# Kernel optimization log

Measured on AMD Instinct MI355X. Metric: run time of the kernel, lower is better.

## Reference

```python
import jax, jax.numpy as jnp
import numpy as np
from jax import lax

EPS_BN = 1e-5
EPS_LN = 1e-5


def setup_inputs() -> dict:
    key = jax.random.key(0)
    ks = jax.random.split(key, 10)
    B, Cin, H, W = 32, 512, 56, 56
    Cout, Cr = 128, 128 // 16  # CBAM reduction 16
    x = jax.random.normal(ks[0], (B, Cin, H, W), dtype=jnp.float32)
    w_proj = jax.random.normal(ks[1], (Cout, Cin), dtype=jnp.float32) * 0.02
    bn_g = jnp.ones((Cout,), jnp.float32)
    bn_b = jnp.zeros((Cout,), jnp.float32)
    bn_m = jax.random.normal(ks[2], (Cout,), dtype=jnp.float32) * 0.1
    bn_v = jax.random.uniform(ks[3], (Cout,), dtype=jnp.float32, minval=0.5, maxval=1.5)
    ca_w1 = jax.random.normal(ks[4], (Cr, Cout), dtype=jnp.float32) * 0.05
    ca_w2 = jax.random.normal(ks[5], (Cout, Cr), dtype=jnp.float32) * 0.05
    sa_w = jax.random.normal(ks[6], (1, 2, 7, 7), dtype=jnp.float32) * 0.05
    ln_g = jnp.ones((Cout,), jnp.float32)
    ln_b = jnp.zeros((Cout,), jnp.float32)
    return dict(x=x, w_proj=w_proj, bn_g=bn_g, bn_b=bn_b, bn_m=bn_m, bn_v=bn_v,
                ca_w1=ca_w1, ca_w2=ca_w2, sa_w=sa_w, ln_g=ln_g, ln_b=ln_b)


def _cbam(x, ca_w1, ca_w2, sa_w):
    # Channel attention: shared MLP on GAP and GMP over spatial dims
    avg = x.mean(axis=(2, 3))  # [B, C]
    mx = x.max(axis=(2, 3))    # [B, C]
    mlp = lambda p: jnp.einsum('cr,br->bc', ca_w2, jax.nn.relu(jnp.einsum('rc,bc->br', ca_w1, p)))
    ca = jax.nn.sigmoid(mlp(avg) + mlp(mx))  # [B, C]
    x = x * ca[:, :, None, None]
    # Spatial attention: channel-wise avg/max -> 7x7 conv -> sigmoid
    s = jnp.stack([x.mean(axis=1), x.max(axis=1)], axis=1)  # [B, 2, H, W]
    sa = lax.conv_general_dilated(s, sa_w, (1, 1), [(3, 3), (3, 3)],
                                  dimension_numbers=('NCHW', 'OIHW', 'NCHW'))
    return x * jax.nn.sigmoid(sa)


def reference(x, w_proj, bn_g, bn_b, bn_m, bn_v, ca_w1, ca_w2, sa_w, ln_g, ln_b):
    # 1x1 conv (no bias) as GEMM over channels
    h = jnp.einsum('bchw,oc->bohw', x, w_proj)
    # BatchNorm (inference) + SiLU
    scale = (bn_g / jnp.sqrt(bn_v + EPS_BN))[None, :, None, None]
    shift = (bn_b - bn_m * bn_g / jnp.sqrt(bn_v + EPS_BN))[None, :, None, None]
    h = h * scale + shift
    h = h * jax.nn.sigmoid(h)  # SiLU
    # CBAM with residual
    y = _cbam(h, ca_w1, ca_w2, sa_w) + h
    # GAP over spatial -> LayerNorm over channels
    y = y.mean(axis=(2, 3))  # [B, C]
    mu = y.mean(axis=-1, keepdims=True)
    var = ((y - mu) ** 2).mean(axis=-1, keepdims=True)
    return (y - mu) / jnp.sqrt(var + EPS_LN) * ln_g + ln_b
```

## Files before the change

kernel.cpp:

```cpp
#include <hip/hip_runtime.h>
#include <hip/hip_bf16.h>

typedef __bf16 bf16x8 __attribute__((ext_vector_type(8)));
typedef float f32x4 __attribute__((ext_vector_type(4)));

#define NB 32
#define CIN 512
#define COUT 128
#define NP 3136
#define WIMG 56

__device__ __forceinline__ unsigned fenc(float f) {
    unsigned u = __float_as_uint(f);
    return (u & 0x80000000u) ? ~u : (u | 0x80000000u);
}
__device__ __forceinline__ float fdec(unsigned e) {
    unsigned u = (e & 0x80000000u) ? (e ^ 0x80000000u) : ~e;
    return __uint_as_float(u);
}
__device__ __forceinline__ float bflo(unsigned u) { return __uint_as_float(u << 16); }
__device__ __forceinline__ float bfhi(unsigned u) { return __uint_as_float(u & 0xffff0000u); }

__device__ __forceinline__ unsigned cvt2_fp8(float a, float b) {
    unsigned r;
    asm volatile("v_cvt_pk_fp8_f32 %0, %1, %2" : "=&v"(r) : "v"(a), "v"(b));
    return r & 0xffffu;
}
__device__ __forceinline__ unsigned pack4_fp8(unsigned u01, unsigned u23) {
    unsigned lo = cvt2_fp8(bflo(u01), bfhi(u01));
    unsigned hi = cvt2_fp8(bflo(u23), bfhi(u23));
    return lo | (hi << 16);
}
__device__ __forceinline__ float fp8_entry(int v) {
    unsigned s = (v >> 7) & 1, e = (v >> 3) & 15, m = v & 7;
    if (e) return __uint_as_float((s << 31) | ((e + 120) << 23) | (m << 20));
    float f = (float)m * 0x1p-9f;
    return s ? -f : f;
}

__device__ __forceinline__ void lds_barrier() {
    asm volatile("s_waitcnt lgkmcnt(0)" ::: "memory");
    __builtin_amdgcn_s_barrier();
    __builtin_amdgcn_sched_barrier(0);
}

__global__ __launch_bounds__(256) void k_wcvt(const float* __restrict__ wp,
                                              ushort* __restrict__ wb,
                                              unsigned* __restrict__ zero8k)
{
    int i = blockIdx.x * 256 + threadIdx.x;
    if (i < 2 * NB * COUT) zero8k[i] = 0u;
    float4 f = *(const float4*)(wp + i * 4);
    ushort4 u;
    __bf16 b0 = (__bf16)f.x, b1 = (__bf16)f.y, b2 = (__bf16)f.z, b3 = (__bf16)f.w;
    u.x = *(ushort*)&b0; u.y = *(ushort*)&b1; u.z = *(ushort*)&b2; u.w = *(ushort*)&b3;
    *(ushort4*)(wb + i * 4) = u;
}

__global__ __launch_bounds__(512, 6) void k_main(
    const float* __restrict__ x, const ushort* __restrict__ wb,
    const float* __restrict__ bn_g, const float* __restrict__ bn_b,
    const float* __restrict__ bn_m, const float* __restrict__ bn_v,
    uchar* __restrict__ hout, float* __restrict__ sumh, unsigned* __restrict__ mxenc)
{
    __shared__ __align__(16) ushort Xs[2][64 * 64];
    __shared__ __align__(16) ushort Ws[2][128 * 64];
    __shared__ float bnss[256];
    __shared__ float redS[2][COUT];
    __shared__ float redM[2][COUT];

    const int bid  = blockIdx.x;
    const int swz  = (bid & 7) * 196 + (bid >> 3);
    const int t    = threadIdx.x;
    const int b    = swz / 49;
    const int p0   = (swz % 49) * 64;
    const int lane = t & 63;
    const int l15  = lane & 15;
    const int lg   = lane >> 4;
    const int w    = t >> 6;
    const int wm   = w >> 1;
    const int wn   = w & 1;

    if (t < COUT) {
        float sc = bn_g[t] * rsqrtf(bn_v[t] + 1e-5f);
        bnss[t]        = sc;
        bnss[t + COUT] = bn_b[t] - bn_m[t] * sc;
    }

    const int pr = t & 63;
    const int kg = t >> 6;
    const float* xb = x + ((size_t)b * CIN) * NP + p0 + pr;
    const int xbyte = pr * 128 + ((kg * 16) ^ ((pr & 7) << 4));

    const int ow = t >> 2, kq = t & 3;
    const ushort* wsrc = wb + ow * CIN + kq * 16;
    const int wbyte0 = ow * 128 + ((kq * 32) ^ ((ow & 7) << 4));
    const int wbyte1 = ow * 128 + ((kq * 32 + 16) ^ ((ow & 7) << 4));

    f32x4 acc[2][2];
#pragma unroll
    for (int mf = 0; mf < 2; ++mf)
#pragma unroll
        for (int nf = 0; nf < 2; ++nf) acc[mf][nf] = (f32x4){0.f, 0.f, 0.f, 0.f};

    float ldx[2][8];
    uint4 ldw0, ldw1;

#pragma unroll
    for (int j = 0; j < 8; ++j) {
        ldx[0][j] = xb[(kg * 8 + j) * NP];
        ldx[1][j] = xb[(64 + kg * 8 + j) * NP];
    }
    ldw0 = *(const uint4*)(wsrc);
    ldw1 = *(const uint4*)(wsrc + 8);
    {
        bf16x8 v8;
#pragma unroll
        for (int j = 0; j < 8; ++j) v8[j] = (__bf16)ldx[0][j];
        *(bf16x8*)((char*)Xs[0] + xbyte) = v8;
        *(uint4*)((char*)Ws[0] + wbyte0) = ldw0;
        *(uint4*)((char*)Ws[0] + wbyte1) = ldw1;
    }

#pragma unroll
    for (int kc = 0; kc < 8; ++kc) {
        lds_barrier();
        if (kc < 6) {
#pragma unroll
            for (int j = 0; j < 8; ++j)
                ldx[kc & 1][j] = xb[((kc + 2) * 64 + kg * 8 + j) * NP];
        }
        if (kc < 7) {
            ldw0 = *(const uint4*)(wsrc + (kc + 1) * 64);
            ldw1 = *(const uint4*)(wsrc + (kc + 1) * 64 + 8);
        }
#pragma unroll
        for (int ks = 0; ks < 2; ++ks) {
            bf16x8 af[2], bfr[2];
#pragma unroll
            for (int mf = 0; mf < 2; ++mf) {
                int o = wm * 32 + mf * 16 + l15;
                af[mf] = *(const bf16x8*)((const char*)Ws[kc & 1]
                          + o * 128 + ((ks * 64 + lg * 16) ^ ((o & 7) << 4)));
            }
#pragma unroll
            for (int nf = 0; nf < 2; ++nf) {
                int p = wn * 32 + nf * 16 + l15;
                bfr[nf] = *(const bf16x8*)((const char*)Xs[kc & 1]
                           + p * 128 + ((ks * 64 + lg * 16) ^ ((p & 7) << 4)));
            }
#pragma unroll
            for (int mf = 0; mf < 2; ++mf)
#pragma unroll
                for (int nf = 0; nf < 2; ++nf)
                    acc[mf][nf] = __builtin_amdgcn_mfma_f32_16x16x32_bf16(
                        af[mf], bfr[nf], acc[mf][nf], 0, 0, 0);
        }
        if (kc < 7) {
            bf16x8 v8;
#pragma unroll
            for (int j = 0; j < 8; ++j) v8[j] = (__bf16)ldx[(kc + 1) & 1][j];
            *(bf16x8*)((char*)Xs[(kc + 1) & 1] + xbyte) = v8;
            *(uint4*)((char*)Ws[(kc + 1) & 1] + wbyte0) = ldw0;
            *(uint4*)((char*)Ws[(kc + 1) & 1] + wbyte1) = ldw1;
        }
    }

    __syncthreads();
    ushort* Hs = (ushort*)Xs;
#pragma unroll
    for (int mf = 0; mf < 2; ++mf) {
#pragma unroll
        for (int reg = 0; reg < 4; ++reg) {
            int o = wm * 32 + mf * 16 + lg * 4 + reg;
            float sc = bnss[o], sh = bnss[o + COUT];
            float s_ = 0.f, m_ = -1e30f;
#pragma unroll
            for (int nf = 0; nf < 2; ++nf) {
                float d    = acc[mf][nf][reg];
                float hval = d * sc + sh;
                hval       = hval / (1.f + __expf(-hval));
                s_ += hval;
                m_ = fmaxf(m_, hval);
                __bf16 hb = (__bf16)hval;
                Hs[o * 64 + wn * 32 + nf * 16 + l15] = *(ushort*)&hb;
            }
#pragma unroll
            for (int d = 1; d < 16; d <<= 1) {
                s_ += __shfl_xor(s_, d, 64);
                m_ = fmaxf(m_, __shfl_xor(m_, d, 64));
            }
            if (l15 == 0) {
                redS[wn][o] = s_;
                redM[wn][o] = m_;
            }
        }
    }
    __syncthreads();
    if (t < COUT) {
        atomicAdd(&sumh[b * COUT + t], redS[0][t] + redS[1][t]);
        atomicMax(&mxenc[b * COUT + t], fenc(fmaxf(redM[0][t], redM[1][t])));
    }
    {
        int orow = t >> 2, c = t & 3;
        uint4 a  = *(const uint4*)&Hs[orow * 64 + c * 16];
        uint4 b4 = *(const uint4*)&Hs[orow * 64 + c * 16 + 8];
        uint4 o4;
        o4.x = pack4_fp8(a.x, a.y);
        o4.y = pack4_fp8(a.z, a.w);
        o4.z = pack4_fp8(b4.x, b4.y);
        o4.w = pack4_fp8(b4.z, b4.w);
        *(uint4*)&hout[((size_t)b * COUT + orow) * NP + p0 + c * 16] = o4;
    }
}

__global__ __launch_bounds__(256) void k_sstat(const uchar* __restrict__ h,
                                               const float* __restrict__ sumh,
                                               const unsigned* __restrict__ mxenc,
                                               const float* __restrict__ w1,
                                               const float* __restrict__ w2,
                                               float* __restrict__ ca,
                                               float* __restrict__ sbuf)
{
    int b = blockIdx.y, z = blockIdx.z;
    int t = threadIdx.x;
    __shared__ float avg[128], mx[128], r1[16], cas[32], tab[256];
    tab[t] = fp8_entry(t);
    if (t < 128) {
        avg[t] = sumh[b * COUT + t] * (1.f / (float)NP);
        mx[t]  = fdec(mxenc[b * COUT + t]);
    }
    __syncthreads();
    if (t < 16) {
        int r = t & 7;
        const float* p = (t < 8) ? avg : mx;
        float s = 0.f;
        for (int c = 0; c < 128; ++c) s += w1[r * 128 + c] * p[c];
        r1[t] = fmaxf(s, 0.f);
    }
    __syncthreads();
    if (t < 32) {
        int o = z * 32 + t;
        float s = 0.f;
#pragma unroll
        for (int r = 0; r < 8; ++r) s += w2[o * 8 + r] * (r1[r] + r1[r + 8]);
        float cv = 1.f / (1.f + __expf(-s));
        cas[t] = cv;
        if (blockIdx.x == 0) ca[b * COUT + o] = cv;
    }
    __syncthreads();

    int idx = blockIdx.x * 256 + t;
    if (idx >= NP / 4) return;
    int p = idx * 4;
    const uchar* hb = h + ((size_t)(b * COUT + z * 32)) * NP + p;
    float s0 = 0.f, s1 = 0.f, s2 = 0.f, s3 = 0.f;
    float m0 = -1e30f, m1 = -1e30f, m2 = -1e30f, m3 = -1e30f;
#pragma unroll 4
    for (int c = 0; c < 32; ++c) {
        unsigned u = *(const unsigned*)(hb + (size_t)c * NP);
        float cv = cas[c];
        float v0 = tab[u & 255] * cv;
        float v1 = tab[(u >> 8) & 255] * cv;
        float v2 = tab[(u >> 16) & 255] * cv;
        float v3 = tab[u >> 24] * cv;
        s0 += v0; s1 += v1; s2 += v2; s3 += v3;
        m0 = fmaxf(m0, v0); m1 = fmaxf(m1, v1);
        m2 = fmaxf(m2, v2); m3 = fmaxf(m3, v3);
    }
    float* sb = sbuf + ((size_t)(z * NB + b) * 2) * NP;
    *(float4*)&sb[p]      = make_float4(s0, s1, s2, s3);
    *(float4*)&sb[NP + p] = make_float4(m0, m1, m2, m3);
}

__global__ __launch_bounds__(256) void k_conv(const float* __restrict__ sbuf,
                                              const float* __restrict__ saw,
                                              float* __restrict__ sigsa)
{
    int band = blockIdx.x, b = blockIdx.y;
    int y0 = band * 7;
    int t = threadIdx.x;
    __shared__ float s[2][13 * WIMG];
    __shared__ float w[98];
    if (t < 98) w[t] = saw[t];
    for (int i = t; i < 13 * WIMG; i += 256) {
        int yy = y0 - 3 + i / WIMG;
        float vs = 0.f, vm = 0.f;
        if (yy >= 0 && yy < WIMG) {
            int p = yy * WIMG + (i % WIMG);
            float ssum = 0.f, smax = -1e30f;
#pragma unroll
            for (int z = 0; z < 4; ++z) {
                const float* sb = sbuf + ((size_t)(z * NB + b) * 2) * NP;
                ssum += sb[p];
                smax = fmaxf(smax, sb[NP + p]);
            }
            vs = ssum * (1.f / (float)COUT);
            vm = smax;
        }
        s[0][i] = vs;
        s[1][i] = vm;
    }
    __syncthreads();
    for (int i = t; i < 7 * WIMG; i += 256) {
        int ly = i / WIMG, px = i % WIMG;
        float a = 0.f;
#pragma unroll
        for (int ch = 0; ch < 2; ++ch) {
#pragma unroll
            for (int dy = 0; dy < 7; ++dy) {
                int li = (ly + dy) * WIMG;
                for (int dx = 0; dx < 7; ++dx) {
                    int xx = px + dx - 3;
                    if (xx < 0 || xx >= WIMG) continue;
                    a += s[ch][li + xx] * w[ch * 49 + dy * 7 + dx];
                }
            }
        }
        sigsa[b * NP + (y0 + ly) * WIMG + px] = 1.f / (1.f + __expf(-a));
    }
}

__global__ __launch_bounds__(256) void k_wsum(const uchar* __restrict__ h,
                                              const float* __restrict__ sigsa,
                                              const float* __restrict__ sumh,
                                              const float* __restrict__ ca,
                                              float* __restrict__ y)
{
    int bo = blockIdx.x;
    int b = bo >> 7;
    int t = threadIdx.x;
    __shared__ float tab[256];
    __shared__ float part[4];
    tab[t] = fp8_entry(t);
    __syncthreads();
    const uchar* hr = h + (size_t)bo * NP;
    const float* sg  = sigsa + (size_t)b * NP;
    float s = 0.f;
#pragma unroll
    for (int i = 0; i < 3; ++i) {
        int q = i * 256 + t;
        unsigned u = *(const unsigned*)(hr + q * 4);
        float4 g = *(const float4*)(sg + q * 4);
        s += tab[u & 255] * g.x + tab[(u >> 8) & 255] * g.y
           + tab[(u >> 16) & 255] * g.z + tab[u >> 24] * g.w;
    }
    if (t < 16) {
        int q = 768 + t;
        unsigned u = *(const unsigned*)(hr + q * 4);
        float4 g = *(const float4*)(sg + q * 4);
        s += tab[u & 255] * g.x + tab[(u >> 8) & 255] * g.y
           + tab[(u >> 16) & 255] * g.z + tab[u >> 24] * g.w;
    }
#pragma unroll
    for (int d = 1; d < 64; d <<= 1) s += __shfl_xor(s, d, 64);
    if ((t & 63) == 0) part[t >> 6] = s;
    __syncthreads();
    if (t == 0) {
        float tt = part[0] + part[1] + part[2] + part[3];
        y[bo] = (sumh[bo] + ca[bo] * tt) * (1.f / (float)NP);
    }
}

__global__ void k_ln(const float* __restrict__ y, const float* __restrict__ g,
                     const float* __restrict__ bta, float* __restrict__ out)
{
    int b = blockIdx.x, t = threadIdx.x;
    __shared__ float pr[2], pr2[2];
    float v = y[b * COUT + t];
    float s = v;
#pragma unroll
    for (int d = 1; d < 64; d <<= 1) s += __shfl_xor(s, d, 64);
    if ((t & 63) == 0) pr[t >> 6] = s;
    __syncthreads();
    float mu = (pr[0] + pr[1]) * (1.f / (float)COUT);
    float dv = v - mu;
    float q = dv * dv;
#pragma unroll
    for (int d = 1; d < 64; d <<= 1) q += __shfl_xor(q, d, 64);
    if ((t & 63) == 0) pr2[t >> 6] = q;
    __syncthreads();
    float var = (pr2[0] + pr2[1]) * (1.f / (float)COUT);
    out[b * COUT + t] = dv * rsqrtf(var + 1e-5f) * g[t] + bta[t];
}

extern "C" void kernel_launch(void* const* d_in, const int* in_sizes, int n_in,
                              void* d_out, int out_size, void* d_ws, size_t ws_size,
                              hipStream_t stream)
{
    const float* x     = (const float*)d_in[0];
    const float* wp    = (const float*)d_in[1];
    const float* bn_g  = (const float*)d_in[2];
    const float* bn_b  = (const float*)d_in[3];
    const float* bn_m  = (const float*)d_in[4];
    const float* bn_v  = (const float*)d_in[5];
    const float* ca_w1 = (const float*)d_in[6];
    const float* ca_w2 = (const float*)d_in[7];
    const float* sa_w  = (const float*)d_in[8];
    const float* ln_g  = (const float*)d_in[9];
    const float* ln_b  = (const float*)d_in[10];
    float* out = (float*)d_out;

    char* ws = (char*)d_ws;
    size_t off = 0;
    uchar*    hbuf  = (uchar*)(ws + off);    off += (size_t)NB * COUT * NP;
    float*    sumh  = (float*)(ws + off);    off += NB * COUT * 4;
    unsigned* mxenc = (unsigned*)(ws + off); off += NB * COUT * 4;
    float*    ca    = (float*)(ws + off);    off += NB * COUT * 4;
    float*    sbuf  = (float*)(ws + off);    off += (size_t)4 * NB * 2 * NP * 4;
    float*    sigsa = (float*)(ws + off);    off += (size_t)NB * NP * 4;
    float*    ybuf  = (float*)(ws + off);    off += NB * COUT * 4;
    ushort*   wb16  = (ushort*)(ws + off);   off += (size_t)COUT * CIN * 2;

    k_wcvt<<<64, 256, 0, stream>>>(wp, wb16, (unsigned*)sumh);
    k_main<<<NB * 49, 512, 0, stream>>>(x, wb16, bn_g, bn_b, bn_m, bn_v, hbuf, sumh, mxenc);
    k_sstat<<<dim3(4, NB, 4), 256, 0, stream>>>(hbuf, sumh, mxenc, ca_w1, ca_w2, ca, sbuf);
    k_conv<<<dim3(8, NB), 256, 0, stream>>>(sbuf, sa_w, sigsa);
    k_wsum<<<NB * COUT, 256, 0, stream>>>(hbuf, sigsa, sumh, ca, ybuf);
    k_ln<<<NB, 128, 0, stream>>>(ybuf, ln_g, ln_b, out);
}
```

Baseline: 79.73 us.

## Switch projection GEMM from bf16 to fp8 MFMA with fp8 weight and activation staging

Weights are converted to fp8 instead of bf16, and input activations are packed to fp8 before going into shared memory. The GEMM then uses the 16x16x32 fp8 MFMA with a 128-wide K chunk, so it runs 4 outer iterations instead of 8. This halves LDS footprint and traffic per K element and the number of barriers. The cost is a large precision loss: the weights (~0.02 magnitude) sit near the bottom of the fp8 e4m3 normal range, and each thread now holds 32 prefetch registers, which can raise register pressure.

```diff
diff --git a/kernel.cpp b/kernel.cpp
--- a/kernel.cpp
+++ b/kernel.cpp
@@ -31,6 +31,9 @@
     unsigned hi = cvt2_fp8(bflo(u23), bfhi(u23));
     return lo | (hi << 16);
 }
+__device__ __forceinline__ unsigned pack4_fp8f(float a, float b, float c, float d) {
+    return cvt2_fp8(a, b) | (cvt2_fp8(c, d) << 16);
+}
 __device__ __forceinline__ float fp8_entry(int v) {
     unsigned s = (v >> 7) & 1, e = (v >> 3) & 15, m = v & 7;
     if (e) return __uint_as_float((s << 31) | ((e + 120) << 23) | (m << 20));
@@ -45,26 +48,23 @@
 }
 
 __global__ __launch_bounds__(256) void k_wcvt(const float* __restrict__ wp,
-                                              ushort* __restrict__ wb,
+                                              unsigned* __restrict__ wf8,
                                               unsigned* __restrict__ zero8k)
 {
     int i = blockIdx.x * 256 + threadIdx.x;
     if (i < 2 * NB * COUT) zero8k[i] = 0u;
     float4 f = *(const float4*)(wp + i * 4);
-    ushort4 u;
-    __bf16 b0 = (__bf16)f.x, b1 = (__bf16)f.y, b2 = (__bf16)f.z, b3 = (__bf16)f.w;
-    u.x = *(ushort*)&b0; u.y = *(ushort*)&b1; u.z = *(ushort*)&b2; u.w = *(ushort*)&b3;
-    *(ushort4*)(wb + i * 4) = u;
+    wf8[i] = pack4_fp8f(f.x, f.y, f.z, f.w);
 }
 
 __global__ __launch_bounds__(512, 6) void k_main(
-    const float* __restrict__ x, const ushort* __restrict__ wb,
+    const float* __restrict__ x, const uchar* __restrict__ wf8,
     const float* __restrict__ bn_g, const float* __restrict__ bn_b,
     const float* __restrict__ bn_m, const float* __restrict__ bn_v,
     uchar* __restrict__ hout, float* __restrict__ sumh, unsigned* __restrict__ mxenc)
 {
-    __shared__ __align__(16) ushort Xs[2][64 * 64];
-    __shared__ __align__(16) ushort Ws[2][128 * 64];
+    __shared__ __align__(16) uchar Xs[2][64 * 128];
+    __shared__ __align__(16) uchar Ws[2][128 * 128];
     __shared__ float bnss[256];
     __shared__ float redS[2][COUT];
     __shared__ float redM[2][COUT];
@@ -93,7 +93,7 @@
     const int xbyte = pr * 128 + ((kg * 16) ^ ((pr & 7) << 4));
 
     const int ow = t >> 2, kq = t & 3;
-    const ushort* wsrc = wb + ow * CIN + kq * 16;
+    const uchar* wsrc = wf8 + ow * CIN + kq * 32;
     const int wbyte0 = ow * 128 + ((kq * 32) ^ ((ow & 7) << 4));
     const int wbyte1 = ow * 128 + ((kq * 32 + 16) ^ ((ow & 7) << 4));
 
@@ -103,66 +103,71 @@
 #pragma unroll
         for (int nf = 0; nf < 2; ++nf) acc[mf][nf] = (f32x4){0.f, 0.f, 0.f, 0.f};
 
-    float ldx[2][8];
+    float ldx[2][16];
     uint4 ldw0, ldw1;
 
 #pragma unroll
-    for (int j = 0; j < 8; ++j) {
-        ldx[0][j] = xb[(kg * 8 + j) * NP];
-        ldx[1][j] = xb[(64 + kg * 8 + j) * NP];
-    }
+    for (int s = 0; s < 2; ++s)
+#pragma unroll
+        for (int j = 0; j < 16; ++j)
+            ldx[s][j] = xb[(s * 128 + kg * 16 + j) * NP];
     ldw0 = *(const uint4*)(wsrc);
-    ldw1 = *(const uint4*)(wsrc + 8);
+    ldw1 = *(const uint4*)(wsrc + 16);
     {
-        bf16x8 v8;
-#pragma unroll
-        for (int j = 0; j < 8; ++j) v8[j] = (__bf16)ldx[0][j];
-        *(bf16x8*)((char*)Xs[0] + xbyte) = v8;
-        *(uint4*)((char*)Ws[0] + wbyte0) = ldw0;
-        *(uint4*)((char*)Ws[0] + wbyte1) = ldw1;
-    }
-
-#pragma unroll
-    for (int kc = 0; kc < 8; ++kc) {
+        uint4 v;
+        v.x = pack4_fp8f(ldx[0][0],  ldx[0][1],  ldx[0][2],  ldx[0][3]);
+        v.y = pack4_fp8f(ldx[0][4],  ldx[0][5],  ldx[0][6],  ldx[0][7]);
+        v.z = pack4_fp8f(ldx[0][8],  ldx[0][9],  ldx[0][10], ldx[0][11]);
+        v.w = pack4_fp8f(ldx[0][12], ldx[0][13], ldx[0][14], ldx[0][15]);
+        *(uint4*)(Xs[0] + xbyte) = v;
+        *(uint4*)(Ws[0] + wbyte0) = ldw0;
+        *(uint4*)(Ws[0] + wbyte1) = ldw1;
+    }
+
+#pragma unroll
+    for (int kc = 0; kc < 4; ++kc) {
         lds_barrier();
-        if (kc < 6) {
-#pragma unroll
-            for (int j = 0; j < 8; ++j)
-                ldx[kc & 1][j] = xb[((kc + 2) * 64 + kg * 8 + j) * NP];
-        }
-        if (kc < 7) {
-            ldw0 = *(const uint4*)(wsrc + (kc + 1) * 64);
-            ldw1 = *(const uint4*)(wsrc + (kc + 1) * 64 + 8);
-        }
-#pragma unroll
-        for (int ks = 0; ks < 2; ++ks) {
-            bf16x8 af[2], bfr[2];
+        if (kc < 2) {
+#pragma unroll
+            for (int j = 0; j < 16; ++j)
+                ldx[kc & 1][j] = xb[((kc + 2) * 128 + kg * 16 + j) * NP];
+        }
+        if (kc < 3) {
+            ldw0 = *(const uint4*)(wsrc + (kc + 1) * 128);
+            ldw1 = *(const uint4*)(wsrc + (kc + 1) * 128 + 16);
+        }
+#pragma unroll
+        for (int ks = 0; ks < 4; ++ks) {
+            long af[2], bfr[2];
 #pragma unroll
             for (int mf = 0; mf < 2; ++mf) {
                 int o = wm * 32 + mf * 16 + l15;
-                af[mf] = *(const bf16x8*)((const char*)Ws[kc & 1]
-                          + o * 128 + ((ks * 64 + lg * 16) ^ ((o & 7) << 4)));
+                af[mf] = *(const long*)(Ws[kc & 1]
+                          + o * 128 + ((ks * 32 + lg * 8) ^ ((o & 7) << 4)));
             }
 #pragma unroll
             for (int nf = 0; nf < 2; ++nf) {
                 int p = wn * 32 + nf * 16 + l15;
-                bfr[nf] = *(const bf16x8*)((const char*)Xs[kc & 1]
-                           + p * 128 + ((ks * 64 + lg * 16) ^ ((p & 7) << 4)));
+                bfr[nf] = *(const long*)(Xs[kc & 1]
+                           + p * 128 + ((ks * 32 + lg * 8) ^ ((p & 7) << 4)));
             }
 #pragma unroll
             for (int mf = 0; mf < 2; ++mf)
 #pragma unroll
                 for (int nf = 0; nf < 2; ++nf)
-                    acc[mf][nf] = __builtin_amdgcn_mfma_f32_16x16x32_bf16(
+                    acc[mf][nf] = __builtin_amdgcn_mfma_f32_16x16x32_fp8_fp8(
                         af[mf], bfr[nf], acc[mf][nf], 0, 0, 0);
         }
-        if (kc < 7) {
-            bf16x8 v8;
-#pragma unroll
-            for (int j = 0; j < 8; ++j) v8[j] = (__bf16)ldx[(kc + 1) & 1][j];
-            *(bf16x8*)((char*)Xs[(kc + 1) & 1] + xbyte) = v8;
-            *(uint4*)((char*)Ws[(kc + 1) & 1] + wbyte0) = ldw0;
-            *(uint4*)((char*)Ws[(kc + 1) & 1] + wbyte1) = ldw1;
+        if (kc < 3) {
+            uint4 v;
+            const float* L = ldx[(kc + 1) & 1];
+            v.x = pack4_fp8f(L[0],  L[1],  L[2],  L[3]);
+            v.y = pack4_fp8f(L[4],  L[5],  L[6],  L[7]);
+            v.z = pack4_fp8f(L[8],  L[9],  L[10], L[11]);
+            v.w = pack4_fp8f(L[12], L[13], L[14], L[15]);
+            *(uint4*)(Xs[(kc + 1) & 1] + xbyte) = v;
+            *(uint4*)(Ws[(kc + 1) & 1] + wbyte0) = ldw0;
+            *(uint4*)(Ws[(kc + 1) & 1] + wbyte1) = ldw1;
         }
     }
 
@@ -410,10 +415,11 @@
     float*    sbuf  = (float*)(ws + off);    off += (size_t)4 * NB * 2 * NP * 4;
     float*    sigsa = (float*)(ws + off);    off += (size_t)NB * NP * 4;
     float*    ybuf  = (float*)(ws + off);    off += NB * COUT * 4;
-    ushort*   wb16  = (ushort*)(ws + off);   off += (size_t)COUT * CIN * 2;
-
-    k_wcvt<<<64, 256, 0, stream>>>(wp, wb16, (unsigned*)sumh);
-    k_main<<<NB * 49, 512, 0, stream>>>(x, wb16, bn_g, bn_b, bn_m, bn_v, hbuf, sumh, mxenc);
+    unsigned* wf8   = (unsigned*)(ws + off); off += (size_t)COUT * CIN;
+
+    k_wcvt<<<64, 256, 0, stream>>>(wp, wf8, (unsigned*)sumh);
+    k_main<<<NB * 49, 512, 0, stream>>>(x, (const uchar*)wf8, bn_g, bn_b, bn_m, bn_v,
+                                        hbuf, sumh, mxenc);
     k_sstat<<<dim3(4, NB, 4), 256, 0, stream>>>(hbuf, sumh, mxenc, ca_w1, ca_w2, ca, sbuf);
     k_conv<<<dim3(8, NB), 256, 0, stream>>>(sbuf, sa_w, sigsa);
     k_wsum<<<NB * COUT, 256, 0, stream>>>(hbuf, sigsa, sumh, ca, ybuf);
```

New measurement: 80.82 us. Within noise of the previous version (+1.4%).

## Fold weight conversion into main kernel and replace atomics with per-strip partials

Applied to the files above, without the earlier changes.

Removes the separate weight-conversion kernel: the main GEMM kernel now loads fp32 weights and converts them to bf16 on the fly while staging into shared memory. The global atomicAdd/atomicMax on per-channel sum and max are replaced by plain stores of per-strip partials, which the stats kernel reduces over 49 strips. This drops one launch and the zeroing pass and avoids atomic contention. In exchange the main kernel reads twice as many weight bytes and does extra conversion work, and the stats kernel does a serial 49-step reduction per channel.

```diff
diff --git a/kernel.cpp b/kernel.cpp
--- a/kernel.cpp
+++ b/kernel.cpp
@@ -10,14 +10,6 @@
 #define NP 3136
 #define WIMG 56
 
-__device__ __forceinline__ unsigned fenc(float f) {
-    unsigned u = __float_as_uint(f);
-    return (u & 0x80000000u) ? ~u : (u | 0x80000000u);
-}
-__device__ __forceinline__ float fdec(unsigned e) {
-    unsigned u = (e & 0x80000000u) ? (e ^ 0x80000000u) : ~e;
-    return __uint_as_float(u);
-}
 __device__ __forceinline__ float bflo(unsigned u) { return __uint_as_float(u << 16); }
 __device__ __forceinline__ float bfhi(unsigned u) { return __uint_as_float(u & 0xffff0000u); }
 
@@ -30,6 +22,10 @@
     unsigned lo = cvt2_fp8(bflo(u01), bfhi(u01));
     unsigned hi = cvt2_fp8(bflo(u23), bfhi(u23));
     return lo | (hi << 16);
+}
+__device__ __forceinline__ unsigned pack2_bf16(float a, float b) {
+    __bf16 x = (__bf16)a, y = (__bf16)b;
+    return (unsigned)*(ushort*)&x | ((unsigned)*(ushort*)&y << 16);
 }
 __device__ __forceinline__ float fp8_entry(int v) {
     unsigned s = (v >> 7) & 1, e = (v >> 3) & 15, m = v & 7;
@@ -44,24 +40,11 @@
     __builtin_amdgcn_sched_barrier(0);
 }
 
-__global__ __launch_bounds__(256) void k_wcvt(const float* __restrict__ wp,
-                                              ushort* __restrict__ wb,
-                                              unsigned* __restrict__ zero8k)
-{
-    int i = blockIdx.x * 256 + threadIdx.x;
-    if (i < 2 * NB * COUT) zero8k[i] = 0u;
-    float4 f = *(const float4*)(wp + i * 4);
-    ushort4 u;
-    __bf16 b0 = (__bf16)f.x, b1 = (__bf16)f.y, b2 = (__bf16)f.z, b3 = (__bf16)f.w;
-    u.x = *(ushort*)&b0; u.y = *(ushort*)&b1; u.z = *(ushort*)&b2; u.w = *(ushort*)&b3;
-    *(ushort4*)(wb + i * 4) = u;
-}
-
 __global__ __launch_bounds__(512, 6) void k_main(
-    const float* __restrict__ x, const ushort* __restrict__ wb,
+    const float* __restrict__ x, const float* __restrict__ wp,
     const float* __restrict__ bn_g, const float* __restrict__ bn_b,
     const float* __restrict__ bn_m, const float* __restrict__ bn_v,
-    uchar* __restrict__ hout, float* __restrict__ sumh, unsigned* __restrict__ mxenc)
+    uchar* __restrict__ hout, float* __restrict__ partS, float* __restrict__ partM)
 {
     __shared__ __align__(16) ushort Xs[2][64 * 64];
     __shared__ __align__(16) ushort Ws[2][128 * 64];
@@ -69,17 +52,18 @@
     __shared__ float redS[2][COUT];
     __shared__ float redM[2][COUT];
 
-    const int bid  = blockIdx.x;
-    const int swz  = (bid & 7) * 196 + (bid >> 3);
-    const int t    = threadIdx.x;
-    const int b    = swz / 49;
-    const int p0   = (swz % 49) * 64;
-    const int lane = t & 63;
-    const int l15  = lane & 15;
-    const int lg   = lane >> 4;
-    const int w    = t >> 6;
-    const int wm   = w >> 1;
-    const int wn   = w & 1;
+    const int bid   = blockIdx.x;
+    const int swz   = (bid & 7) * 196 + (bid >> 3);
+    const int t     = threadIdx.x;
+    const int b     = swz / 49;
+    const int strip = swz % 49;
+    const int p0    = strip * 64;
+    const int lane  = t & 63;
+    const int l15   = lane & 15;
+    const int lg    = lane >> 4;
+    const int w     = t >> 6;
+    const int wm    = w >> 1;
+    const int wn    = w & 1;
 
     if (t < COUT) {
         float sc = bn_g[t] * rsqrtf(bn_v[t] + 1e-5f);
@@ -93,7 +77,7 @@
     const int xbyte = pr * 128 + ((kg * 16) ^ ((pr & 7) << 4));
 
     const int ow = t >> 2, kq = t & 3;
-    const ushort* wsrc = wb + ow * CIN + kq * 16;
+    const float* wsrcf = wp + ow * CIN + kq * 16;
     const int wbyte0 = ow * 128 + ((kq * 32) ^ ((ow & 7) << 4));
     const int wbyte1 = ow * 128 + ((kq * 32 + 16) ^ ((ow & 7) << 4));
 
@@ -104,22 +88,31 @@
         for (int nf = 0; nf < 2; ++nf) acc[mf][nf] = (f32x4){0.f, 0.f, 0.f, 0.f};
 
     float ldx[2][8];
-    uint4 ldw0, ldw1;
+    float ldwf[16];
 
 #pragma unroll
     for (int j = 0; j < 8; ++j) {
         ldx[0][j] = xb[(kg * 8 + j) * NP];
         ldx[1][j] = xb[(64 + kg * 8 + j) * NP];
     }
-    ldw0 = *(const uint4*)(wsrc);
-    ldw1 = *(const uint4*)(wsrc + 8);
+#pragma unroll
+    for (int q = 0; q < 4; ++q) {
+        float4 f = *(const float4*)(wsrcf + q * 4);
+        ldwf[q * 4 + 0] = f.x; ldwf[q * 4 + 1] = f.y;
+        ldwf[q * 4 + 2] = f.z; ldwf[q * 4 + 3] = f.w;
+    }
     {
         bf16x8 v8;
 #pragma unroll
         for (int j = 0; j < 8; ++j) v8[j] = (__bf16)ldx[0][j];
         *(bf16x8*)((char*)Xs[0] + xbyte) = v8;
-        *(uint4*)((char*)Ws[0] + wbyte0) = ldw0;
-        *(uint4*)((char*)Ws[0] + wbyte1) = ldw1;
+        uint4 wv0, wv1;
+        wv0.x = pack2_bf16(ldwf[0],  ldwf[1]);  wv0.y = pack2_bf16(ldwf[2],  ldwf[3]);
+        wv0.z = pack2_bf16(ldwf[4],  ldwf[5]);  wv0.w = pack2_bf16(ldwf[6],  ldwf[7]);
+        wv1.x = pack2_bf16(ldwf[8],  ldwf[9]);  wv1.y = pack2_bf16(ldwf[10], ldwf[11]);
+        wv1.z = pack2_bf16(ldwf[12], ldwf[13]); wv1.w = pack2_bf16(ldwf[14], ldwf[15]);
+        *(uint4*)((char*)Ws[0] + wbyte0) = wv0;
+        *(uint4*)((char*)Ws[0] + wbyte1) = wv1;
     }
 
 #pragma unroll
@@ -131,8 +124,12 @@
                 ldx[kc & 1][j] = xb[((kc + 2) * 64 + kg * 8 + j) * NP];
         }
         if (kc < 7) {
-            ldw0 = *(const uint4*)(wsrc + (kc + 1) * 64);
-            ldw1 = *(const uint4*)(wsrc + (kc + 1) * 64 + 8);
+#pragma unroll
+            for (int q = 0; q < 4; ++q) {
+                float4 f = *(const float4*)(wsrcf + (kc + 1) * 64 + q * 4);
+                ldwf[q * 4 + 0] = f.x; ldwf[q * 4 + 1] = f.y;
+                ldwf[q * 4 + 2] = f.z; ldwf[q * 4 + 3] = f.w;
+            }
         }
 #pragma unroll
         for (int ks = 0; ks < 2; ++ks) {
@@ -161,8 +158,13 @@
 #pragma unroll
             for (int j = 0; j < 8; ++j) v8[j] = (__bf16)ldx[(kc + 1) & 1][j];
             *(bf16x8*)((char*)Xs[(kc + 1) & 1] + xbyte) = v8;
-            *(uint4*)((char*)Ws[(kc + 1) & 1] + wbyte0) = ldw0;
-            *(uint4*)((char*)Ws[(kc + 1) & 1] + wbyte1) = ldw1;
+            uint4 wv0, wv1;
+            wv0.x = pack2_bf16(ldwf[0],  ldwf[1]);  wv0.y = pack2_bf16(ldwf[2],  ldwf[3]);
+            wv0.z = pack2_bf16(ldwf[4],  ldwf[5]);  wv0.w = pack2_bf16(ldwf[6],  ldwf[7]);
+            wv1.x = pack2_bf16(ldwf[8],  ldwf[9]);  wv1.y = pack2_bf16(ldwf[10], ldwf[11]);
+            wv1.z = pack2_bf16(ldwf[12], ldwf[13]); wv1.w = pack2_bf16(ldwf[14], ldwf[15]);
+            *(uint4*)((char*)Ws[(kc + 1) & 1] + wbyte0) = wv0;
+            *(uint4*)((char*)Ws[(kc + 1) & 1] + wbyte1) = wv1;
         }
     }
 
@@ -198,8 +200,9 @@
     }
     __syncthreads();
     if (t < COUT) {
-        atomicAdd(&sumh[b * COUT + t], redS[0][t] + redS[1][t]);
-        atomicMax(&mxenc[b * COUT + t], fenc(fmaxf(redM[0][t], redM[1][t])));
+        size_t pidx = ((size_t)strip * NB + b) * COUT + t;
+        partS[pidx] = redS[0][t] + redS[1][t];
+        partM[pidx] = fmaxf(redM[0][t], redM[1][t]);
     }
     {
         int orow = t >> 2, c = t & 3;
@@ -215,11 +218,12 @@
 }
 
 __global__ __launch_bounds__(256) void k_sstat(const uchar* __restrict__ h,
-                                               const float* __restrict__ sumh,
-                                               const unsigned* __restrict__ mxenc,
+                                               const float* __restrict__ partS,
+                                               const float* __restrict__ partM,
                                                const float* __restrict__ w1,
                                                const float* __restrict__ w2,
                                                float* __restrict__ ca,
+                                               float* __restrict__ sumtot,
                                                float* __restrict__ sbuf)
 {
     int b = blockIdx.y, z = blockIdx.z;
@@ -227,8 +231,15 @@
     __shared__ float avg[128], mx[128], r1[16], cas[32], tab[256];
     tab[t] = fp8_entry(t);
     if (t < 128) {
-        avg[t] = sumh[b * COUT + t] * (1.f / (float)NP);
-        mx[t]  = fdec(mxenc[b * COUT + t]);
+        float s = 0.f, m = -1e30f;
+        for (int sp = 0; sp < 49; ++sp) {
+            size_t pidx = ((size_t)sp * NB + b) * COUT + t;
+            s += partS[pidx];
+            m = fmaxf(m, partM[pidx]);
+        }
+        if (blockIdx.x == 0 && z == 0) sumtot[b * COUT + t] = s;
+        avg[t] = s * (1.f / (float)NP);
+        mx[t]  = m;
     }
     __syncthreads();
     if (t < 16) {
@@ -323,7 +334,7 @@
 
 __global__ __launch_bounds__(256) void k_wsum(const uchar* __restrict__ h,
                                               const float* __restrict__ sigsa,
-                                              const float* __restrict__ sumh,
+                                              const float* __restrict__ sumtot,
                                               const float* __restrict__ ca,
                                               float* __restrict__ y)
 {
@@ -358,7 +369,7 @@
     __syncthreads();
     if (t == 0) {
         float tt = part[0] + part[1] + part[2] + part[3];
-        y[bo] = (sumh[bo] + ca[bo] * tt) * (1.f / (float)NP);
+        y[bo] = (sumtot[bo] + ca[bo] * tt) * (1.f / (float)NP);
     }
 }
 
@@ -404,18 +415,17 @@
     char* ws = (char*)d_ws;
     size_t off = 0;
     uchar*    hbuf  = (uchar*)(ws + off);    off += (size_t)NB * COUT * NP;
-    float*    sumh  = (float*)(ws + off);    off += NB * COUT * 4;
-    unsigned* mxenc = (unsigned*)(ws + off); off += NB * COUT * 4;
+    float*    partS = (float*)(ws + off);    off += (size_t)49 * NB * COUT * 4;
+    float*    partM = (float*)(ws + off);    off += (size_t)49 * NB * COUT * 4;
+    float*    sumtot= (float*)(ws + off);    off += NB * COUT * 4;
     float*    ca    = (float*)(ws + off);    off += NB * COUT * 4;
     float*    sbuf  = (float*)(ws + off);    off += (size_t)4 * NB * 2 * NP * 4;
     float*    sigsa = (float*)(ws + off);    off += (size_t)NB * NP * 4;
     float*    ybuf  = (float*)(ws + off);    off += NB * COUT * 4;
-    ushort*   wb16  = (ushort*)(ws + off);   off += (size_t)COUT * CIN * 2;
-
-    k_wcvt<<<64, 256, 0, stream>>>(wp, wb16, (unsigned*)sumh);
-    k_main<<<NB * 49, 512, 0, stream>>>(x, wb16, bn_g, bn_b, bn_m, bn_v, hbuf, sumh, mxenc);
-    k_sstat<<<dim3(4, NB, 4), 256, 0, stream>>>(hbuf, sumh, mxenc, ca_w1, ca_w2, ca, sbuf);
+
+    k_main<<<NB * 49, 512, 0, stream>>>(x, wp, bn_g, bn_b, bn_m, bn_v, hbuf, partS, partM);
+    k_sstat<<<dim3(4, NB, 4), 256, 0, stream>>>(hbuf, partS, partM, ca_w1, ca_w2, ca, sumtot, sbuf);
     k_conv<<<dim3(8, NB), 256, 0, stream>>>(sbuf, sa_w, sigsa);
-    k_wsum<<<NB * COUT, 256, 0, stream>>>(hbuf, sigsa, sumh, ca, ybuf);
+    k_wsum<<<NB * COUT, 256, 0, stream>>>(hbuf, sigsa, sumtot, ca, ybuf);
     k_ln<<<NB, 128, 0, stream>>>(ybuf, ln_g, ln_b, out);
 }
```

After: 83.54 us. 1.05x slower.
